# Performance work log

Measured on AMD Instinct MI355X. Metric: run time of the kernel, lower is better.

## Reference

```python
import jax, jax.numpy as jnp
import numpy as np

B, L, F = 4096, 50, 128      # batch, hist_l, per-step feature dim (in_dim // hist_l)
H, E = 8, 128                # h_att, emb_dim
DQK = E                      # per-head q/k dim = (emb_dim*h_att)//h_att
DV = E // H                  # per-head v dim = emb_dim // h_att


def setup_inputs() -> dict:
    key = jax.random.key(0)
    ks = jax.random.split(key, 7)
    s_f = 1.0 / np.sqrt(F)
    return {
        "hid": jax.random.normal(ks[0], (B, L * F), dtype=jnp.float32),
        "Wq": jax.random.normal(ks[1], (H, F, DQK), dtype=jnp.float32) * s_f,
        "bq": jax.random.normal(ks[2], (H, DQK), dtype=jnp.float32) * 0.01,
        "Wk": jax.random.normal(ks[3], (H, F, DQK), dtype=jnp.float32) * s_f,
        "bk": jax.random.normal(ks[4], (H, DQK), dtype=jnp.float32) * 0.01,
        "Wv": jax.random.normal(ks[5], (H, F, DV), dtype=jnp.float32) * s_f,
        "bv": jax.random.normal(ks[6], (H, DV), dtype=jnp.float32) * 0.01,
    }


def reference(hid, Wq, bq, Wk, bk, Wv, bv):
    b = hid.shape[0]
    x = hid.reshape(b, L, F)                                   # [B, L, F]
    # all heads batched: q,k [B, H, L, DQK], v [B, H, L, DV]
    q = jnp.einsum("blf,hfe->bhle", x, Wq) + bq[None, :, None, :]
    k = jnp.einsum("blf,hfe->bhle", x, Wk) + bk[None, :, None, :]
    v = jnp.einsum("blf,hfv->bhlv", x, Wv) + bv[None, :, None, :]
    scores = jnp.einsum("bhle,bhme->bhlm", q, k)               # [B, H, L, L]
    scores = jnp.where(scores > 0, scores, 0.1 * scores)       # leaky_relu(0.1)
    # original uses nn.Softmax(dim=1) on [B, L, L] -> normalize over ROW axis (axis 2 here)
    att = jax.nn.softmax(scores, axis=2)
    out = jnp.einsum("bhlm,bhmv->bhlv", att, v)                # [B, H, L, DV]
    out = jnp.transpose(out, (0, 2, 1, 3)).reshape(b, L, H * DV)  # concat heads last-dim
    return jax.nn.relu(out).reshape(b, -1)                     # [B, L*emb_dim]
```

## Files before the change

kernel.cpp:

```cpp
#include <hip/hip_runtime.h>
#include <math.h>

#define NB   4096
#define LL   50
#define FF   128
#define HH   8
#define DVn  16

typedef __attribute__((ext_vector_type(8))) short bf16x8;
typedef __attribute__((ext_vector_type(4))) float f32x4;

__device__ __forceinline__ ushort bf_hi(float x) {
    uint u = __float_as_uint(x);
    uint r = u + 0x7FFFu + ((u >> 16) & 1u);
    return (ushort)(r >> 16);
}
__device__ __forceinline__ float bf_f(ushort b) { return __uint_as_float(((uint)b) << 16); }

__global__ __launch_bounds__(64)
void pack_w(const float* __restrict__ Wq, const float* __restrict__ bq,
            const float* __restrict__ Wk, const float* __restrict__ bk,
            const float* __restrict__ Wv, ushort* __restrict__ wp)
{
    __shared__ float sw[48*129];
    const int lane = threadIdx.x;
    const int bx   = blockIdx.x;
    const int h    = bx / 40;
    const int r40  = bx % 40;
    const int tile = r40 >> 2;
    const int ks   = r40 & 3;
    const int c    = lane & 15;
    const int quad = lane >> 4;
    const int f0   = ks*32 + quad*8;

    float val[8];
    #pragma unroll
    for (int j = 0; j < 8; ++j) val[j] = 0.f;

    if (tile < 8) {
        const float* wq = Wq + (size_t)h*FF*FF;
        const float* wk = Wk + (size_t)h*FF*FF;
        float* wqs = sw;
        float* wks = sw + 16*129;
        for (int i = lane; i < 16*128; i += 64)
            wqs[(i>>7)*129 + (i&127)] = wq[(size_t)(tile*16 + (i>>7))*FF + (i&127)];
        for (int i = lane; i < 32*128; i += 64)
            wks[(i>>7)*129 + (i&127)] = wk[(size_t)(ks*32 + (i>>7))*FF + (i&127)];
        __syncthreads();
        for (int e = 0; e < FF; ++e) {
            float qv = wqs[c*129 + e];
            #pragma unroll
            for (int j = 0; j < 8; ++j)
                val[j] += wks[(quad*8 + j)*129 + e] * qv;
        }
    } else if (tile == 8) {
        const float* wq = Wq + (size_t)h*FF*FF;
        const float* wk = Wk + (size_t)h*FF*FF;
        float pu[8], pv[8];
        #pragma unroll
        for (int j = 0; j < 8; ++j) { pu[j] = 0.f; pv[j] = 0.f; }
        for (int ee = 0; ee < 8; ++ee) {
            int e = c*8 + ee;
            float bkk = bk[h*FF + e], bqq = bq[h*FF + e];
            #pragma unroll
            for (int j = 0; j < 8; ++j) {
                pu[j] += wq[(size_t)(f0+j)*FF + e] * bkk;
                pv[j] += wk[(size_t)(f0+j)*FF + e] * bqq;
            }
        }
        #pragma unroll
        for (int m = 1; m < 16; m <<= 1) {
            #pragma unroll
            for (int j = 0; j < 8; ++j) {
                pu[j] += __shfl_xor(pu[j], m);
                pv[j] += __shfl_xor(pv[j], m);
            }
        }
        if (c == 0) {
            #pragma unroll
            for (int j = 0; j < 8; ++j) val[j] = pu[j];
        } else if (c == 1) {
            #pragma unroll
            for (int j = 0; j < 8; ++j) val[j] = pv[j];
        }
        if (ks == 0) {
            float s = bq[h*FF + lane*2]*bk[h*FF + lane*2]
                    + bq[h*FF + lane*2 + 1]*bk[h*FF + lane*2 + 1];
            #pragma unroll
            for (int m = 1; m < 64; m <<= 1) s += __shfl_xor(s, m);
            if (lane == 0) ((float*)(wp + 327680))[h] = s;
        }
    } else {
        const float* wv = Wv + (size_t)h*FF*DVn;
        #pragma unroll
        for (int j = 0; j < 8; ++j) val[j] = wv[(size_t)(f0+j)*DVn + c];
    }

    ushort hi[8], lo[8];
    #pragma unroll
    for (int j = 0; j < 8; ++j) {
        ushort hb = bf_hi(val[j]);
        hi[j] = hb;
        lo[j] = bf_hi(val[j] - bf_f(hb));
    }
    size_t base = (size_t)h*40960 + (size_t)tile*4096 + ks*1024 + lane*8;
    *(ushort4*)(wp + base)       = make_ushort4(hi[0],hi[1],hi[2],hi[3]);
    *(ushort4*)(wp + base + 4)   = make_ushort4(hi[4],hi[5],hi[6],hi[7]);
    *(ushort4*)(wp + base + 512) = make_ushort4(lo[0],lo[1],lo[2],lo[3]);
    *(ushort4*)(wp + base + 516) = make_ushort4(lo[4],lo[5],lo[6],lo[7]);
}

#define PX    528
#define XL0   0
#define XH0   8448
#define GB0   8448
#define GDEL  8448
#define SATT0 8448
#define SATTP 88
#define VF0   25344
#define TU0   13184
#define TV0   13248
#define LDS_FLOATS 13312

__global__ __launch_bounds__(256, 3)
void attn_fused(const float* __restrict__ hid, const ushort* __restrict__ wp,
                const float* __restrict__ ccp, const float* __restrict__ bv,
                float* __restrict__ out)
{
    __shared__ __align__(16) float lds[LDS_FLOATS];
    ushort* us = (ushort*)lds;
    float*  tu = lds + TU0;
    float*  tv = lds + TV0;

    const int t    = threadIdx.x;
    const int b    = blockIdx.x;
    const int lane = t & 63;
    const int w    = t >> 6;
    const int c16  = lane & 15;
    const int quad = lane >> 4;

    {
        const float4* src = (const float4*)(hid + (size_t)b * (LL*FF));
        for (int i = t; i < 1600; i += 256) {
            float4 v = src[i];
            int l = i >> 5, f0 = (i & 31) * 4;
            int slot = ((l>>4)*4 + (f0>>5))*PX + ((l&15) + 16*((f0&31)>>3))*8 + (f0&7);
            ushort4 hv, lv;
            uint ux;
            ux = __float_as_uint(v.x); hv.x = (ushort)(ux>>16);
            lv.x = (ushort)(__float_as_uint(v.x - __uint_as_float(ux & 0xFFFF0000u))>>16);
            ux = __float_as_uint(v.y); hv.y = (ushort)(ux>>16);
            lv.y = (ushort)(__float_as_uint(v.y - __uint_as_float(ux & 0xFFFF0000u))>>16);
            ux = __float_as_uint(v.z); hv.z = (ushort)(ux>>16);
            lv.z = (ushort)(__float_as_uint(v.z - __uint_as_float(ux & 0xFFFF0000u))>>16);
            ux = __float_as_uint(v.w); hv.w = (ushort)(ux>>16);
            lv.w = (ushort)(__float_as_uint(v.w - __uint_as_float(ux & 0xFFFF0000u))>>16);
            *(ushort4*)(us + XH0 + slot) = hv;
            *(ushort4*)(us + XL0 + slot) = lv;
        }
    }
    __syncthreads();

    bf16x8 xh[16];
    #pragma unroll
    for (int i = 0; i < 16; ++i)
        xh[i] = *(const bf16x8*)(us + XH0 + i*PX + lane*8);
    __syncthreads();

    #pragma unroll 1
    for (int h = 0; h < HH; ++h) {
        f32x4 aG[2][4], aU, aV;
        #pragma unroll
        for (int i = 0; i < 2; ++i)
            #pragma unroll
            for (int m = 0; m < 4; ++m) aG[i][m] = (f32x4){0.f,0.f,0.f,0.f};
        aU = (f32x4){0.f,0.f,0.f,0.f};
        aV = (f32x4){0.f,0.f,0.f,0.f};

        const ushort* wb = wp + (size_t)h*40960 + lane*8;
        #define WFRG(tt,kk,pp) (*(const bf16x8*)(wb + (size_t)(tt)*4096 + (kk)*1024 + (pp)*512))

        #pragma unroll
        for (int ks = 0; ks < 4; ++ks) {
            bf16x8 m0h = WFRG(2*w,   ks, 0), m0l = WFRG(2*w,   ks, 1);
            bf16x8 m1h = WFRG(2*w+1, ks, 0), m1l = WFRG(2*w+1, ks, 1);
            bf16x8 uvh = WFRG(8, ks, 0);
            bf16x8 vvh = WFRG(9, ks, 0);
            #pragma unroll
            for (int mt = 0; mt < 4; ++mt) {
                bf16x8 bh = xh[mt*4 + ks];
                bf16x8 bl = *(const bf16x8*)(us + XL0 + (mt*4 + ks)*PX + lane*8);
                aG[0][mt] = __builtin_amdgcn_mfma_f32_16x16x32_bf16(m0h, bh, aG[0][mt], 0,0,0);
                aG[0][mt] = __builtin_amdgcn_mfma_f32_16x16x32_bf16(m0l, bh, aG[0][mt], 0,0,0);
                aG[0][mt] = __builtin_amdgcn_mfma_f32_16x16x32_bf16(m0h, bl, aG[0][mt], 0,0,0);
                aG[1][mt] = __builtin_amdgcn_mfma_f32_16x16x32_bf16(m1h, bh, aG[1][mt], 0,0,0);
                aG[1][mt] = __builtin_amdgcn_mfma_f32_16x16x32_bf16(m1l, bh, aG[1][mt], 0,0,0);
                aG[1][mt] = __builtin_amdgcn_mfma_f32_16x16x32_bf16(m1h, bl, aG[1][mt], 0,0,0);
                if (mt == w) {
                    aU = __builtin_amdgcn_mfma_f32_16x16x32_bf16(bh, uvh, aU, 0,0,0);
                    aV = __builtin_amdgcn_mfma_f32_16x16x32_bf16(bh, vvh, aV, 0,0,0);
                    aV = __builtin_amdgcn_mfma_f32_16x16x32_bf16(bl, vvh, aV, 0,0,0);
                }
            }
        }

        {
            #pragma unroll
            for (int i = 0; i < 2; ++i) {
                #pragma unroll
                for (int mt = 0; mt < 4; ++mt) {
                    uint u0 = __float_as_uint(aG[i][mt][0]);
                    uint u1 = __float_as_uint(aG[i][mt][1]);
                    uint u2 = __float_as_uint(aG[i][mt][2]);
                    uint u3 = __float_as_uint(aG[i][mt][3]);
                    uint hw0 = (u0>>16) | (u1 & 0xFFFF0000u);
                    uint hw1 = (u2>>16) | (u3 & 0xFFFF0000u);
                    float l0 = aG[i][mt][0] - __uint_as_float(u0 & 0xFFFF0000u);
                    float l1 = aG[i][mt][1] - __uint_as_float(u1 & 0xFFFF0000u);
                    float l2 = aG[i][mt][2] - __uint_as_float(u2 & 0xFFFF0000u);
                    float l3 = aG[i][mt][3] - __uint_as_float(u3 & 0xFFFF0000u);
                    uint lw0 = (__float_as_uint(l0)>>16) | (__float_as_uint(l1) & 0xFFFF0000u);
                    uint lw1 = (__float_as_uint(l2)>>16) | (__float_as_uint(l3) & 0xFFFF0000u);
                    ushort* dst = us + GB0 + (mt*4 + w)*PX
                                  + (c16 + 16*(2*i + (quad>>1)))*8 + (quad&1)*4;
                    *(uint2*)dst          = make_uint2(hw0, hw1);
                    *(uint2*)(dst + GDEL) = make_uint2(lw0, lw1);
                }
            }
            if (c16 < 2) {
                float* dst = (c16 == 0) ? tu : tv;
                #pragma unroll
                for (int r = 0; r < 4; ++r) dst[w*16 + quad*4 + r] = aU[r];
            }
            float bvv = bv[h*DVn + c16];
            int ksp = w >> 1;
            #pragma unroll
            for (int r = 0; r < 4; ++r) {
                int m  = w*16 + quad*4 + r;
                int mm = (w&1)*16 + quad*4 + r;
                int Lp = c16 + 16*(mm >> 3);
                us[VF0 + ksp*512 + Lp*8 + (mm & 7)] = (m < LL) ? bf_hi(aV[r] + bvv) : (ushort)0;
            }
        }
        __syncthreads();

        f32x4 sc[4];
        #pragma unroll
        for (int m = 0; m < 4; ++m) sc[m] = (f32x4){0.f,0.f,0.f,0.f};

        #pragma unroll
        for (int ks = 0; ks < 4; ++ks) {
            const ushort* gb = us + GB0 + (w*4 + ks)*PX + lane*8;
            bf16x8 gh = *(const bf16x8*)gb;
            bf16x8 gl = *(const bf16x8*)(gb + GDEL);
            #pragma unroll
            for (int mt = 0; mt < 4; ++mt) {
                bf16x8 ah = xh[mt*4 + ks];
                bf16x8 al = *(const bf16x8*)(us + XL0 + (mt*4 + ks)*PX + lane*8);
                sc[mt] = __builtin_amdgcn_mfma_f32_16x16x32_bf16(ah, gh, sc[mt], 0,0,0);
                sc[mt] = __builtin_amdgcn_mfma_f32_16x16x32_bf16(al, gh, sc[mt], 0,0,0);
                sc[mt] = __builtin_amdgcn_mfma_f32_16x16x32_bf16(ah, gl, sc[mt], 0,0,0);
            }
        }

        const float cc  = ccp[h];
        const int mcol  = w*16 + c16;
        const float tvv = tv[mcol] + cc;
        float mx = -INFINITY;
        #pragma unroll
        for (int mt = 0; mt < 4; ++mt) {
            const float4 tq = *(const float4*)(tu + mt*16 + quad*4);
            float tqa[4] = {tq.x, tq.y, tq.z, tq.w};
            #pragma unroll
            for (int r = 0; r < 4; ++r) {
                int l = mt*16 + quad*4 + r;
                float s = sc[mt][r] + tqa[r] + tvv;
                s = (s > 0.f) ? s : 0.1f*s;
                sc[mt][r] = s;
                if (l < LL) mx = fmaxf(mx, s);
            }
        }
        mx = fmaxf(mx, __shfl_xor(mx, 16));
        mx = fmaxf(mx, __shfl_xor(mx, 32));
        float sum = 0.f;
        #pragma unroll
        for (int mt = 0; mt < 4; ++mt)
            #pragma unroll
            for (int r = 0; r < 4; ++r) {
                int l = mt*16 + quad*4 + r;
                float p = (l < LL) ? __expf(sc[mt][r] - mx) : 0.f;
                sc[mt][r] = p;
                sum += p;
            }
        sum += __shfl_xor(sum, 16);
        sum += __shfl_xor(sum, 32);
        float inv = 1.0f / sum;

        __syncthreads();

        #pragma unroll
        for (int mt = 0; mt < 4; ++mt)
            #pragma unroll
            for (int r = 0; r < 4; ++r) {
                int l = mt*16 + quad*4 + r;
                us[SATT0 + l*SATTP + mcol] = (mcol < LL) ? bf_hi(sc[mt][r] * inv) : (ushort)0;
            }
        __syncthreads();

        f32x4 ao = (f32x4){0.f,0.f,0.f,0.f};
        #pragma unroll
        for (int ksp = 0; ksp < 2; ++ksp) {
            bf16x8 af = *(const bf16x8*)(us + SATT0 + (w*16 + c16)*SATTP + ksp*32 + quad*8);
            bf16x8 bf = *(const bf16x8*)(us + VF0 + ksp*512 + lane*8);
            ao = __builtin_amdgcn_mfma_f32_16x16x32_bf16(af, bf, ao, 0,0,0);
        }
        #pragma unroll
        for (int r = 0; r < 4; ++r) {
            int l = w*16 + quad*4 + r;
            if (l < LL)
                out[(size_t)b*(LL*FF) + l*FF + h*DVn + c16] = fmaxf(ao[r], 0.f);
        }
        __syncthreads();
    }
}

extern "C" void kernel_launch(void* const* d_in, const int* in_sizes, int n_in,
                              void* d_out, int out_size, void* d_ws, size_t ws_size,
                              hipStream_t stream)
{
    const float* hid = (const float*)d_in[0];
    const float* Wq  = (const float*)d_in[1];
    const float* bq  = (const float*)d_in[2];
    const float* Wk  = (const float*)d_in[3];
    const float* bk  = (const float*)d_in[4];
    const float* Wv  = (const float*)d_in[5];
    const float* bv  = (const float*)d_in[6];
    float* o    = (float*)d_out;
    ushort* wp  = (ushort*)d_ws;
    const float* ccp = (const float*)(wp + 327680);

    pack_w<<<dim3(320), dim3(64), 0, stream>>>(Wq, bq, Wk, bk, Wv, wp);
    attn_fused<<<dim3(NB), dim3(256), 0, stream>>>(hid, wp, ccp, bv, o);
}
```

Before: 478.7 us.

## Split per-head G computation into halves to shrink LDS and raise occupancy

The attention kernel now computes the folded Wq·Wk^T product G in two halves per head. Each half is staged into a smaller LDS buffer and immediately consumed by the score MFMAs. This drops the row padding (PX 528→512), cuts the LDS footprint from about 53KB to about 35KB, and raises launch bounds to 4 blocks per CU to hide latency. In exchange it adds an extra barrier per half, and the unpadded layout may cause LDS bank conflicts. The weight packing kernel is also restructured to use 256-thread blocks that load the full Wk once per block.

```diff
diff --git a/kernel.cpp b/kernel.cpp
--- a/kernel.cpp
+++ b/kernel.cpp
@@ -17,18 +17,17 @@
 }
 __device__ __forceinline__ float bf_f(ushort b) { return __uint_as_float(((uint)b) << 16); }
 
-__global__ __launch_bounds__(64)
+__global__ __launch_bounds__(256)
 void pack_w(const float* __restrict__ Wq, const float* __restrict__ bq,
             const float* __restrict__ Wk, const float* __restrict__ bk,
             const float* __restrict__ Wv, ushort* __restrict__ wp)
 {
-    __shared__ float sw[48*129];
-    const int lane = threadIdx.x;
-    const int bx   = blockIdx.x;
-    const int h    = bx / 40;
-    const int r40  = bx % 40;
-    const int tile = r40 >> 2;
-    const int ks   = r40 & 3;
+    __shared__ float sw[144*129];
+    const int t    = threadIdx.x;
+    const int lane = t & 63;
+    const int ks   = t >> 6;
+    const int h    = blockIdx.x / 10;
+    const int tile = blockIdx.x % 10;
     const int c    = lane & 15;
     const int quad = lane >> 4;
     const int f0   = ks*32 + quad*8;
@@ -42,16 +41,17 @@
         const float* wk = Wk + (size_t)h*FF*FF;
         float* wqs = sw;
         float* wks = sw + 16*129;
-        for (int i = lane; i < 16*128; i += 64)
+        for (int i = t; i < 16*128; i += 256)
             wqs[(i>>7)*129 + (i&127)] = wq[(size_t)(tile*16 + (i>>7))*FF + (i&127)];
-        for (int i = lane; i < 32*128; i += 64)
-            wks[(i>>7)*129 + (i&127)] = wk[(size_t)(ks*32 + (i>>7))*FF + (i&127)];
+        for (int i = t; i < 128*128; i += 256)
+            wks[(i>>7)*129 + (i&127)] = wk[i];
         __syncthreads();
+        const int g0 = ks*32 + quad*8;
         for (int e = 0; e < FF; ++e) {
             float qv = wqs[c*129 + e];
             #pragma unroll
             for (int j = 0; j < 8; ++j)
-                val[j] += wks[(quad*8 + j)*129 + e] * qv;
+                val[j] += wks[(g0+j)*129 + e] * qv;
         }
     } else if (tile == 8) {
         const float* wq = Wq + (size_t)h*FF*FF;
@@ -110,19 +110,18 @@
     *(ushort4*)(wp + base + 516) = make_ushort4(lo[4],lo[5],lo[6],lo[7]);
 }
 
-#define PX    528
 #define XL0   0
-#define XH0   8448
-#define GB0   8448
-#define GDEL  8448
-#define SATT0 8448
+#define XH0   8192
+#define GH0   8192
+#define GLD   4096
+#define SATT0 8192
 #define SATTP 88
-#define VF0   25344
-#define TU0   13184
-#define TV0   13248
-#define LDS_FLOATS 13312
-
-__global__ __launch_bounds__(256, 3)
+#define VF0   16384
+#define TU0   8704
+#define TV0   8768
+#define LDS_FLOATS 8832
+
+__global__ __launch_bounds__(256, 4)
 void attn_fused(const float* __restrict__ hid, const ushort* __restrict__ wp,
                 const float* __restrict__ ccp, const float* __restrict__ bv,
                 float* __restrict__ out)
@@ -144,7 +143,7 @@
         for (int i = t; i < 1600; i += 256) {
             float4 v = src[i];
             int l = i >> 5, f0 = (i & 31) * 4;
-            int slot = ((l>>4)*4 + (f0>>5))*PX + ((l&15) + 16*((f0&31)>>3))*8 + (f0&7);
+            int slot = ((l>>4)*4 + (f0>>5))*512 + ((l&15) + 16*((f0&31)>>3))*8 + (f0&7);
             ushort4 hv, lv;
             uint ux;
             ux = __float_as_uint(v.x); hv.x = (ushort)(ux>>16);
@@ -164,103 +163,108 @@
     bf16x8 xh[16];
     #pragma unroll
     for (int i = 0; i < 16; ++i)
-        xh[i] = *(const bf16x8*)(us + XH0 + i*PX + lane*8);
+        xh[i] = *(const bf16x8*)(us + XH0 + i*512 + lane*8);
     __syncthreads();
 
     #pragma unroll 1
     for (int h = 0; h < HH; ++h) {
-        f32x4 aG[2][4], aU, aV;
-        #pragma unroll
-        for (int i = 0; i < 2; ++i)
-            #pragma unroll
-            for (int m = 0; m < 4; ++m) aG[i][m] = (f32x4){0.f,0.f,0.f,0.f};
+        const ushort* wb = wp + (size_t)h*40960 + lane*8;
+        #define WFRG(tt,kk,pp) (*(const bf16x8*)(wb + (size_t)(tt)*4096 + (kk)*1024 + (pp)*512))
+
+        f32x4 sc[4], aU, aV;
+        #pragma unroll
+        for (int m = 0; m < 4; ++m) sc[m] = (f32x4){0.f,0.f,0.f,0.f};
         aU = (f32x4){0.f,0.f,0.f,0.f};
         aV = (f32x4){0.f,0.f,0.f,0.f};
 
-        const ushort* wb = wp + (size_t)h*40960 + lane*8;
-        #define WFRG(tt,kk,pp) (*(const bf16x8*)(wb + (size_t)(tt)*4096 + (kk)*1024 + (pp)*512))
-
-        #pragma unroll
-        for (int ks = 0; ks < 4; ++ks) {
-            bf16x8 m0h = WFRG(2*w,   ks, 0), m0l = WFRG(2*w,   ks, 1);
-            bf16x8 m1h = WFRG(2*w+1, ks, 0), m1l = WFRG(2*w+1, ks, 1);
-            bf16x8 uvh = WFRG(8, ks, 0);
-            bf16x8 vvh = WFRG(9, ks, 0);
-            #pragma unroll
-            for (int mt = 0; mt < 4; ++mt) {
-                bf16x8 bh = xh[mt*4 + ks];
-                bf16x8 bl = *(const bf16x8*)(us + XL0 + (mt*4 + ks)*PX + lane*8);
-                aG[0][mt] = __builtin_amdgcn_mfma_f32_16x16x32_bf16(m0h, bh, aG[0][mt], 0,0,0);
-                aG[0][mt] = __builtin_amdgcn_mfma_f32_16x16x32_bf16(m0l, bh, aG[0][mt], 0,0,0);
-                aG[0][mt] = __builtin_amdgcn_mfma_f32_16x16x32_bf16(m0h, bl, aG[0][mt], 0,0,0);
-                aG[1][mt] = __builtin_amdgcn_mfma_f32_16x16x32_bf16(m1h, bh, aG[1][mt], 0,0,0);
-                aG[1][mt] = __builtin_amdgcn_mfma_f32_16x16x32_bf16(m1l, bh, aG[1][mt], 0,0,0);
-                aG[1][mt] = __builtin_amdgcn_mfma_f32_16x16x32_bf16(m1h, bl, aG[1][mt], 0,0,0);
-                if (mt == w) {
-                    aU = __builtin_amdgcn_mfma_f32_16x16x32_bf16(bh, uvh, aU, 0,0,0);
-                    aV = __builtin_amdgcn_mfma_f32_16x16x32_bf16(bh, vvh, aV, 0,0,0);
-                    aV = __builtin_amdgcn_mfma_f32_16x16x32_bf16(bl, vvh, aV, 0,0,0);
-                }
-            }
-        }
-
-        {
-            #pragma unroll
-            for (int i = 0; i < 2; ++i) {
+        #pragma unroll
+        for (int hf = 0; hf < 2; ++hf) {
+            f32x4 aG[4];
+            #pragma unroll
+            for (int m = 0; m < 4; ++m) aG[m] = (f32x4){0.f,0.f,0.f,0.f};
+            const int ft = 4*hf + w;
+
+            #pragma unroll
+            for (int ksg = 0; ksg < 4; ++ksg) {
+                bf16x8 mh = WFRG(ft, ksg, 0), ml = WFRG(ft, ksg, 1);
                 #pragma unroll
                 for (int mt = 0; mt < 4; ++mt) {
-                    uint u0 = __float_as_uint(aG[i][mt][0]);
-                    uint u1 = __float_as_uint(aG[i][mt][1]);
-                    uint u2 = __float_as_uint(aG[i][mt][2]);
-                    uint u3 = __float_as_uint(aG[i][mt][3]);
+                    bf16x8 bh = xh[mt*4 + ksg];
+                    bf16x8 bl = *(const bf16x8*)(us + XL0 + (mt*4 + ksg)*512 + lane*8);
+                    aG[mt] = __builtin_amdgcn_mfma_f32_16x16x32_bf16(mh, bh, aG[mt], 0,0,0);
+                    aG[mt] = __builtin_amdgcn_mfma_f32_16x16x32_bf16(ml, bh, aG[mt], 0,0,0);
+                    aG[mt] = __builtin_amdgcn_mfma_f32_16x16x32_bf16(mh, bl, aG[mt], 0,0,0);
+                }
+            }
+            #pragma unroll
+            for (int kb = 0; kb < 2; ++kb) {
+                const int ksf = 2*hf + kb;
+                bf16x8 uvh = WFRG(8, ksf, 0), vvh = WFRG(9, ksf, 0);
+                bf16x8 bhx = xh[w*4 + ksf];
+                bf16x8 blx = *(const bf16x8*)(us + XL0 + (w*4 + ksf)*512 + lane*8);
+                aU = __builtin_amdgcn_mfma_f32_16x16x32_bf16(bhx, uvh, aU, 0,0,0);
+                aV = __builtin_amdgcn_mfma_f32_16x16x32_bf16(bhx, vvh, aV, 0,0,0);
+                aV = __builtin_amdgcn_mfma_f32_16x16x32_bf16(blx, vvh, aV, 0,0,0);
+            }
+
+            {
+                const int pkb  = w >> 1;
+                const int grp  = c16 + 16*(2*(w&1) + (quad>>1));
+                const int joff = (quad&1)*4;
+                #pragma unroll
+                for (int mt = 0; mt < 4; ++mt) {
+                    uint u0 = __float_as_uint(aG[mt][0]);
+                    uint u1 = __float_as_uint(aG[mt][1]);
+                    uint u2 = __float_as_uint(aG[mt][2]);
+                    uint u3 = __float_as_uint(aG[mt][3]);
                     uint hw0 = (u0>>16) | (u1 & 0xFFFF0000u);
                     uint hw1 = (u2>>16) | (u3 & 0xFFFF0000u);
-                    float l0 = aG[i][mt][0] - __uint_as_float(u0 & 0xFFFF0000u);
-                    float l1 = aG[i][mt][1] - __uint_as_float(u1 & 0xFFFF0000u);
-                    float l2 = aG[i][mt][2] - __uint_as_float(u2 & 0xFFFF0000u);
-                    float l3 = aG[i][mt][3] - __uint_as_float(u3 & 0xFFFF0000u);
+                    float l0 = aG[mt][0] - __uint_as_float(u0 & 0xFFFF0000u);
+                    float l1 = aG[mt][1] - __uint_as_float(u1 & 0xFFFF0000u);
+                    float l2 = aG[mt][2] - __uint_as_float(u2 & 0xFFFF0000u);
+                    float l3 = aG[mt][3] - __uint_as_float(u3 & 0xFFFF0000u);
                     uint lw0 = (__float_as_uint(l0)>>16) | (__float_as_uint(l1) & 0xFFFF0000u);
                     uint lw1 = (__float_as_uint(l2)>>16) | (__float_as_uint(l3) & 0xFFFF0000u);
-                    ushort* dst = us + GB0 + (mt*4 + w)*PX
-                                  + (c16 + 16*(2*i + (quad>>1)))*8 + (quad&1)*4;
-                    *(uint2*)dst          = make_uint2(hw0, hw1);
-                    *(uint2*)(dst + GDEL) = make_uint2(lw0, lw1);
+                    ushort* dst = us + GH0 + (mt*2 + pkb)*512 + grp*8 + joff;
+                    *(uint2*)dst         = make_uint2(hw0, hw1);
+                    *(uint2*)(dst + GLD) = make_uint2(lw0, lw1);
                 }
-            }
-            if (c16 < 2) {
-                float* dst = (c16 == 0) ? tu : tv;
+                if (hf == 1) {
+                    if (c16 < 2) {
+                        float* dst = (c16 == 0) ? tu : tv;
+                        #pragma unroll
+                        for (int r = 0; r < 4; ++r) dst[w*16 + quad*4 + r] = aU[r];
+                    }
+                    float bvv = bv[h*DVn + c16];
+                    int ksp = w >> 1;
+                    #pragma unroll
+                    for (int r = 0; r < 4; ++r) {
+                        int m  = w*16 + quad*4 + r;
+                        int mm = (w&1)*16 + quad*4 + r;
+                        int Lp = c16 + 16*(mm >> 3);
+                        us[VF0 + ksp*512 + Lp*8 + (mm & 7)] = (m < LL) ? bf_hi(aV[r] + bvv)
+                                                                       : (ushort)0;
+                    }
+                }
+            }
+            __syncthreads();
+
+            #pragma unroll
+            for (int kb = 0; kb < 2; ++kb) {
+                const int ks = 2*hf + kb;
+                const ushort* gb = us + GH0 + (w*2 + kb)*512 + lane*8;
+                bf16x8 gh = *(const bf16x8*)gb;
+                bf16x8 gl = *(const bf16x8*)(gb + GLD);
                 #pragma unroll
-                for (int r = 0; r < 4; ++r) dst[w*16 + quad*4 + r] = aU[r];
-            }
-            float bvv = bv[h*DVn + c16];
-            int ksp = w >> 1;
-            #pragma unroll
-            for (int r = 0; r < 4; ++r) {
-                int m  = w*16 + quad*4 + r;
-                int mm = (w&1)*16 + quad*4 + r;
-                int Lp = c16 + 16*(mm >> 3);
-                us[VF0 + ksp*512 + Lp*8 + (mm & 7)] = (m < LL) ? bf_hi(aV[r] + bvv) : (ushort)0;
-            }
-        }
-        __syncthreads();
-
-        f32x4 sc[4];
-        #pragma unroll
-        for (int m = 0; m < 4; ++m) sc[m] = (f32x4){0.f,0.f,0.f,0.f};
-
-        #pragma unroll
-        for (int ks = 0; ks < 4; ++ks) {
-            const ushort* gb = us + GB0 + (w*4 + ks)*PX + lane*8;
-            bf16x8 gh = *(const bf16x8*)gb;
-            bf16x8 gl = *(const bf16x8*)(gb + GDEL);
-            #pragma unroll
-            for (int mt = 0; mt < 4; ++mt) {
-                bf16x8 ah = xh[mt*4 + ks];
-                bf16x8 al = *(const bf16x8*)(us + XL0 + (mt*4 + ks)*PX + lane*8);
-                sc[mt] = __builtin_amdgcn_mfma_f32_16x16x32_bf16(ah, gh, sc[mt], 0,0,0);
-                sc[mt] = __builtin_amdgcn_mfma_f32_16x16x32_bf16(al, gh, sc[mt], 0,0,0);
-                sc[mt] = __builtin_amdgcn_mfma_f32_16x16x32_bf16(ah, gl, sc[mt], 0,0,0);
-            }
+                for (int mt = 0; mt < 4; ++mt) {
+                    bf16x8 ah = xh[mt*4 + ks];
+                    bf16x8 al = *(const bf16x8*)(us + XL0 + (mt*4 + ks)*512 + lane*8);
+                    sc[mt] = __builtin_amdgcn_mfma_f32_16x16x32_bf16(ah, gh, sc[mt], 0,0,0);
+                    sc[mt] = __builtin_amdgcn_mfma_f32_16x16x32_bf16(al, gh, sc[mt], 0,0,0);
+                    sc[mt] = __builtin_amdgcn_mfma_f32_16x16x32_bf16(ah, gl, sc[mt], 0,0,0);
+                }
+            }
+            __syncthreads();
         }
 
         const float cc  = ccp[h];
@@ -295,8 +299,6 @@
         sum += __shfl_xor(sum, 16);
         sum += __shfl_xor(sum, 32);
         float inv = 1.0f / sum;
-
-        __syncthreads();
 
         #pragma unroll
         for (int mt = 0; mt < 4; ++mt)
@@ -339,6 +341,6 @@
     ushort* wp  = (ushort*)d_ws;
     const float* ccp = (const float*)(wp + 327680);
 
-    pack_w<<<dim3(320), dim3(64), 0, stream>>>(Wq, bq, Wk, bk, Wv, wp);
+    pack_w<<<dim3(80), dim3(256), 0, stream>>>(Wq, bq, Wk, bk, Wv, wp);
     attn_fused<<<dim3(NB), dim3(256), 0, stream>>>(hid, wp, ccp, bv, o);
 }
```

After: 1.095 ms. 129% more time.
